# Performance work log

Hardware: AMD Instinct MI355X
Metric: run time of the kernel (lower is better)

The kernel has to match this reference:

```python
import jax, jax.numpy as jnp
import numpy as np

N, K, D, E = 30000, 20, 128, 600000


def time_encode(t, w, b):
    # TGN TimeEncode: cos(Linear(1->D)(t)) ; t: [...], returns [..., D]
    return jnp.cos(t[..., None] * w + b)


def setup_inputs() -> dict:
    key = jax.random.key(0)
    ks = jax.random.split(key, 8)
    node_features = jax.random.normal(ks[0], (N, D), dtype=jnp.float32)
    timestamps = jax.random.uniform(ks[1], (N,), dtype=jnp.float32) * 1e4
    edge_features = jax.random.normal(ks[2], (E, D), dtype=jnp.float32)
    neighbors = jax.random.randint(ks[3], (N, K), 0, N, dtype=jnp.int32)
    edge_idxs = jax.random.randint(ks[4], (N, K), 0, E, dtype=jnp.int32)
    # edge interaction times precede the query timestamps (temporal neighbor sampling)
    edge_times = jax.random.uniform(ks[5], (N, K), dtype=jnp.float32) * timestamps[:, None]
    # TGN basis-frequency init for the time encoder
    time_w = (1.0 / 10.0 ** np.linspace(0, 9, D)).astype(np.float32)
    time_w = jnp.asarray(time_w)
    time_b = jnp.zeros((D,), dtype=jnp.float32)
    s1 = 1.0 / np.sqrt(3 * D)
    W1 = jax.random.normal(ks[6], (3 * D, D), dtype=jnp.float32) * s1
    b1 = jnp.zeros((D,), dtype=jnp.float32)
    W2 = jax.random.normal(ks[7], (3 * D, D), dtype=jnp.float32) * s1
    b2 = jnp.zeros((D,), dtype=jnp.float32)
    return {"node_features": node_features, "timestamps": timestamps,
            "edge_features": edge_features, "neighbors": neighbors,
            "edge_idxs": edge_idxs, "edge_times": edge_times,
            "time_w": time_w, "time_b": time_b,
            "W1": W1, "b1": b1, "W2": W2, "b2": b2}


def reference(node_features, timestamps, edge_features, neighbors, edge_idxs,
              edge_times, time_w, time_b, W1, b1, W2, b2):
    # layer-0 neighbor embeddings = raw node features gathered at neighbor ids
    neigh_feat = node_features[neighbors]                       # [N, K, D]
    # time deltas between query time and edge times, then cosine time encoding
    deltas = timestamps[:, None] - edge_times                   # [N, K]
    edge_time_emb = time_encode(deltas, time_w, time_b)         # [N, K, D]
    edge_feat = edge_features[edge_idxs]                        # [N, K, D]
    # GraphSumEmbedding.aggregate
    neighbors_features = jnp.concatenate(
        [neigh_feat, edge_time_emb, edge_feat], axis=-1)        # [N, K, 3D]
    h = neighbors_features @ W1 + b1                            # [N, K, D]
    neighbors_sum = jax.nn.relu(jnp.sum(h, axis=1))             # [N, D]
    src_time_emb = time_encode(jnp.zeros_like(timestamps), time_w, time_b)  # [N, D]
    source_features = jnp.concatenate([node_features, src_time_emb], axis=1)
    source_embedding = jnp.concatenate([neighbors_sum, source_features], axis=1)
    return source_embedding @ W2 + b2                           # [N, D]
```

## Files before the change

### kernel.cpp

```cpp
#include <hip/hip_runtime.h>
#include <math.h>

#define DD 128
#define KNB 20
#define K3 384
#define NPB 8

typedef unsigned short u16;
typedef __attribute__((ext_vector_type(8))) short short8;
typedef __attribute__((ext_vector_type(4))) float f32x4;

static __device__ __forceinline__ u16 f2bf(float x) {
    union { float f; unsigned u; } v; v.f = x;
    unsigned r = v.u + 0x7fffu + ((v.u >> 16) & 1u);
    return (u16)(r >> 16);
}

static __device__ __forceinline__ float fcos(float x) {
    float r = x * 0.15915494309189535f;
    r = __builtin_amdgcn_fractf(r);
    return __builtin_amdgcn_cosf(r);
}

static __device__ __forceinline__ void st4bf(u16* p, float4 v) {
    ushort4 s;
    s.x = f2bf(v.x); s.y = f2bf(v.y); s.z = f2bf(v.z); s.w = f2bf(v.w);
    *(ushort4*)p = s;
}

__global__ __launch_bounds__(DD) void const_kernel(
    const float* __restrict__ tb, const float* __restrict__ W2,
    const float* __restrict__ b2, float* __restrict__ cvec)
{
    int d = threadIdx.x;
    float acc = b2[d];
    #pragma unroll 8
    for (int i = 0; i < DD; ++i)
        acc = fmaf(cosf(tb[i]), W2[(size_t)(2 * DD + i) * DD + d], acc);
    cvec[d] = acc;
}

__global__ __launch_bounds__(256) void pack_w(
    const float* __restrict__ W1, const float* __restrict__ W2,
    u16* __restrict__ W1p, u16* __restrict__ W2p)
{
    int t = blockIdx.x * 256 + threadIdx.x;
    if (t < 6144) {
        int L = t & 63;
        int ct = (t >> 6) & 7;
        int kt = t >> 9;
        int n  = ct * 16 + (L & 15);
        int kb = kt * 32 + (L >> 4) * 8;
        u16* d = W1p + (size_t)t * 8;
        #pragma unroll
        for (int j = 0; j < 8; ++j) d[j] = f2bf(W1[(size_t)(kb + j) * DD + n]);
    } else if (t < 10240) {
        int u = t - 6144;
        int L = u & 63;
        int ct = (u >> 6) & 7;
        int kt = (u >> 9) & 3;
        int part = u >> 11;
        int n  = ct * 16 + (L & 15);
        int kb = part * DD + kt * 32 + (L >> 4) * 8;
        u16* d = W2p + (size_t)u * 8;
        #pragma unroll
        for (int j = 0; j < 8; ++j) d[j] = f2bf(W2[(size_t)(kb + j) * DD + n]);
    }
}

__global__ __launch_bounds__(256) void agg_kernel(
    const float* __restrict__ nodef, const float* __restrict__ ts,
    const float* __restrict__ edgef, const int* __restrict__ neighbors,
    const int* __restrict__ edge_idxs, const float* __restrict__ edge_times,
    const float* __restrict__ tw, const float* __restrict__ tb,
    u16* __restrict__ aggbf, u16* __restrict__ nfbf, int N)
{
    __shared__ int   s_nb[NPB * KNB];
    __shared__ int   s_eg[NPB * KNB];
    __shared__ float s_dt[NPB * KNB];

    const int tid = threadIdx.x;
    const int n0  = blockIdx.x * NPB;

    if (tid < NPB * KNB) {
        int nsub = tid / KNB;
        int k    = tid - nsub * KNB;
        int nn   = n0 + nsub;
        if (nn < N) {
            s_nb[tid] = neighbors[(size_t)nn * KNB + k];
            s_eg[tid] = edge_idxs[(size_t)nn * KNB + k];
            s_dt[tid] = ts[nn] - edge_times[(size_t)nn * KNB + k];
        } else {
            s_nb[tid] = 0; s_eg[tid] = 0; s_dt[tid] = 0.f;
        }
    }
    __syncthreads();

    const int c    = tid & 31;
    const int nsub = tid >> 5;
    const int n    = n0 + nsub;

    const float4* nf4 = (const float4*)nodef;
    const float4* ef4 = (const float4*)edgef;
    const float4  w4  = ((const float4*)tw)[c];
    const float4  b4  = ((const float4*)tb)[c];

    float4 an = make_float4(0.f, 0.f, 0.f, 0.f);
    float4 ae = an, at = an;

    const int*   nb  = s_nb + nsub * KNB;
    const int*   eg  = s_eg + nsub * KNB;
    const float* dtp = s_dt + nsub * KNB;

    #pragma unroll 10
    for (int k = 0; k < KNB; ++k) {
        int   ni = nb[k];
        int   ei = eg[k];
        float dt = dtp[k];
        float4 nv = nf4[(size_t)ni * 32 + c];
        float4 ev = ef4[(size_t)ei * 32 + c];
        an.x += nv.x; an.y += nv.y; an.z += nv.z; an.w += nv.w;
        ae.x += ev.x; ae.y += ev.y; ae.z += ev.z; ae.w += ev.w;
        at.x += fcos(fmaf(dt, w4.x, b4.x));
        at.y += fcos(fmaf(dt, w4.y, b4.y));
        at.z += fcos(fmaf(dt, w4.z, b4.z));
        at.w += fcos(fmaf(dt, w4.w, b4.w));
    }

    if (n < N) {
        u16* o = aggbf + (size_t)n * K3;
        st4bf(o + 4 * c,           an);
        st4bf(o + DD + 4 * c,      at);
        st4bf(o + 2 * DD + 4 * c,  ae);
        float4 sf = nf4[(size_t)n * 32 + c];
        st4bf(nfbf + (size_t)n * DD + 4 * c, sf);
    }
}

#define APITCH 392
#define HPITCH 136

__global__ __launch_bounds__(256) void fused_gemm(
    const u16* __restrict__ aggbf, const u16* __restrict__ nfbf,
    const u16* __restrict__ W1p, const u16* __restrict__ W2p,
    const float* __restrict__ b1, const float* __restrict__ cvec,
    float* __restrict__ out, int N)
{
    __shared__ __align__(16) u16 As[32 * APITCH];

    const int tid  = threadIdx.x;
    const int lane = tid & 63;
    const int wave = tid >> 6;
    const int row0 = blockIdx.x * 32;
    const int m0     = (wave & 1) * 16;
    const int ctbase = (wave >> 1) * 4;
    const int l15  = lane & 15;
    const int quad = lane >> 4;

    {
        const float4* ag4 = (const float4*)aggbf;
        #pragma unroll
        for (int i = 0; i < 6; ++i) {
            int idx = tid + i * 256;
            int r = idx / 48, c = idx - r * 48;
            float4 v = make_float4(0.f, 0.f, 0.f, 0.f);
            int row = row0 + r;
            if (row < N) v = ag4[(size_t)row * 48 + c];
            *(float4*)&As[r * APITCH + c * 8] = v;
        }
    }
    __syncthreads();

    f32x4 acc[4];
    #pragma unroll
    for (int c = 0; c < 4; ++c) acc[c] = (f32x4){0.f, 0.f, 0.f, 0.f};

    const short8* W1v = (const short8*)W1p;
    for (int kt = 0; kt < 12; ++kt) {
        short8 a = *(const short8*)&As[(m0 + l15) * APITCH + kt * 32 + quad * 8];
        #pragma unroll
        for (int c = 0; c < 4; ++c) {
            short8 b = W1v[(size_t)(kt * 8 + ctbase + c) * 64 + lane];
            acc[c] = __builtin_amdgcn_mfma_f32_16x16x32_bf16(a, b, acc[c], 0, 0, 0);
        }
    }
    __syncthreads();

    u16* Hs  = As;
    u16* NFs = As + 32 * HPITCH;
    #pragma unroll
    for (int c = 0; c < 4; ++c) {
        int col = (ctbase + c) * 16 + l15;
        float bb = (float)KNB * b1[col];
        #pragma unroll
        for (int r = 0; r < 4; ++r) {
            float h = acc[c][r] + bb;
            h = h > 0.f ? h : 0.f;
            Hs[(m0 + quad * 4 + r) * HPITCH + col] = f2bf(h);
        }
    }
    {
        const float4* nf4 = (const float4*)nfbf;
        #pragma unroll
        for (int i = 0; i < 2; ++i) {
            int idx = tid + i * 256;
            int r = idx >> 4, c = idx & 15;
            float4 v = make_float4(0.f, 0.f, 0.f, 0.f);
            int row = row0 + r;
            if (row < N) v = nf4[(size_t)row * 16 + c];
            *(float4*)&NFs[r * HPITCH + c * 8] = v;
        }
    }
    __syncthreads();

    f32x4 acc2[4];
    #pragma unroll
    for (int c = 0; c < 4; ++c) {
        float cv = cvec[(ctbase + c) * 16 + l15];
        acc2[c] = (f32x4){cv, cv, cv, cv};
    }
    const short8* W2v = (const short8*)W2p;
    for (int kt = 0; kt < 4; ++kt) {
        short8 aH = *(const short8*)&Hs[(m0 + l15) * HPITCH + kt * 32 + quad * 8];
        #pragma unroll
        for (int c = 0; c < 4; ++c) {
            short8 b = W2v[(size_t)(kt * 8 + ctbase + c) * 64 + lane];
            acc2[c] = __builtin_amdgcn_mfma_f32_16x16x32_bf16(aH, b, acc2[c], 0, 0, 0);
        }
        short8 aN = *(const short8*)&NFs[(m0 + l15) * HPITCH + kt * 32 + quad * 8];
        #pragma unroll
        for (int c = 0; c < 4; ++c) {
            short8 b = W2v[(size_t)((4 + kt) * 8 + ctbase + c) * 64 + lane];
            acc2[c] = __builtin_amdgcn_mfma_f32_16x16x32_bf16(aN, b, acc2[c], 0, 0, 0);
        }
    }

    #pragma unroll
    for (int c = 0; c < 4; ++c) {
        int col = (ctbase + c) * 16 + l15;
        #pragma unroll
        for (int r = 0; r < 4; ++r) {
            int row = row0 + m0 + quad * 4 + r;
            if (row < N) out[(size_t)row * DD + col] = acc2[c][r];
        }
    }
}

extern "C" void kernel_launch(void* const* d_in, const int* in_sizes, int n_in,
                              void* d_out, int out_size, void* d_ws, size_t ws_size,
                              hipStream_t stream)
{
    const float* nodef      = (const float*)d_in[0];
    const float* ts         = (const float*)d_in[1];
    const float* edgef      = (const float*)d_in[2];
    const int*   neighbors  = (const int*)d_in[3];
    const int*   edge_idxs  = (const int*)d_in[4];
    const float* edge_times = (const float*)d_in[5];
    const float* tw         = (const float*)d_in[6];
    const float* tb         = (const float*)d_in[7];
    const float* W1         = (const float*)d_in[8];
    const float* b1         = (const float*)d_in[9];
    const float* W2         = (const float*)d_in[10];
    const float* b2         = (const float*)d_in[11];
    float*       out        = (float*)d_out;

    const int N = in_sizes[1];

    u16*   aggbf = (u16*)d_ws;
    u16*   nfbf  = aggbf + (size_t)N * K3;
    u16*   W1p   = nfbf + (size_t)N * DD;
    u16*   W2p   = W1p + 12 * 8 * 64 * 8;
    float* cvec  = (float*)(W2p + 2 * 4 * 8 * 64 * 8);

    hipLaunchKernelGGL(const_kernel, dim3(1), dim3(DD), 0, stream,
                       tb, W2, b2, cvec);
    hipLaunchKernelGGL(pack_w, dim3(40), dim3(256), 0, stream,
                       W1, W2, W1p, W2p);
    hipLaunchKernelGGL(agg_kernel, dim3((N + NPB - 1) / NPB), dim3(256), 0, stream,
                       nodef, ts, edgef, neighbors, edge_idxs, edge_times,
                       tw, tb, aggbf, nfbf, N);
    hipLaunchKernelGGL(fused_gemm, dim3((N + 31) / 32), dim3(256), 0, stream,
                       aggbf, nfbf, W1p, W2p, b1, cvec, out, N);
}
```

Before: 480.4 us.

## Fuse neighbor aggregation into GEMM kernel and merge weight-prep launches

The gather/aggregation stage now runs inside the GEMM kernel, writing bf16 aggregated rows straight into shared memory instead of a global workspace. The separate constant and pack kernels are merged into one launch. This removes the global round trip of the aggregated buffer and the node-feature copy, plus two launches. In exchange each block does 32 nodes of gather work before its MFMAs, and the grid shrinks from about 3750 to about 940 blocks, so there is less parallelism to hide gather latency.

```diff
diff --git a/kernel.cpp b/kernel.cpp
--- a/kernel.cpp
+++ b/kernel.cpp
@@ -4,7 +4,8 @@
 #define DD 128
 #define KNB 20
 #define K3 384
-#define NPB 8
+#define APITCH 392
+#define HPITCH 136
 
 typedef unsigned short u16;
 typedef __attribute__((ext_vector_type(8))) short short8;
@@ -28,22 +29,22 @@
     *(ushort4*)p = s;
 }
 
-__global__ __launch_bounds__(DD) void const_kernel(
-    const float* __restrict__ tb, const float* __restrict__ W2,
-    const float* __restrict__ b2, float* __restrict__ cvec)
+__global__ __launch_bounds__(256) void prep_kernel(
+    const float* __restrict__ W1, const float* __restrict__ W2,
+    const float* __restrict__ tb, const float* __restrict__ b2,
+    u16* __restrict__ W1p, u16* __restrict__ W2p, float* __restrict__ cvec)
 {
-    int d = threadIdx.x;
-    float acc = b2[d];
-    #pragma unroll 8
-    for (int i = 0; i < DD; ++i)
-        acc = fmaf(cosf(tb[i]), W2[(size_t)(2 * DD + i) * DD + d], acc);
-    cvec[d] = acc;
-}
-
-__global__ __launch_bounds__(256) void pack_w(
-    const float* __restrict__ W1, const float* __restrict__ W2,
-    u16* __restrict__ W1p, u16* __restrict__ W2p)
-{
+    if (blockIdx.x == 40) {
+        int d = threadIdx.x;
+        if (d < DD) {
+            float acc = b2[d];
+            #pragma unroll 8
+            for (int i = 0; i < DD; ++i)
+                acc = fmaf(cosf(tb[i]), W2[(size_t)(2 * DD + i) * DD + d], acc);
+            cvec[d] = acc;
+        }
+        return;
+    }
     int t = blockIdx.x * 256 + threadIdx.x;
     if (t < 6144) {
         int L = t & 63;
@@ -68,109 +69,82 @@
     }
 }
 
-__global__ __launch_bounds__(256) void agg_kernel(
+__global__ __launch_bounds__(256) void fused_all(
     const float* __restrict__ nodef, const float* __restrict__ ts,
     const float* __restrict__ edgef, const int* __restrict__ neighbors,
     const int* __restrict__ edge_idxs, const float* __restrict__ edge_times,
     const float* __restrict__ tw, const float* __restrict__ tb,
-    u16* __restrict__ aggbf, u16* __restrict__ nfbf, int N)
-{
-    __shared__ int   s_nb[NPB * KNB];
-    __shared__ int   s_eg[NPB * KNB];
-    __shared__ float s_dt[NPB * KNB];
-
-    const int tid = threadIdx.x;
-    const int n0  = blockIdx.x * NPB;
-
-    if (tid < NPB * KNB) {
-        int nsub = tid / KNB;
-        int k    = tid - nsub * KNB;
-        int nn   = n0 + nsub;
-        if (nn < N) {
-            s_nb[tid] = neighbors[(size_t)nn * KNB + k];
-            s_eg[tid] = edge_idxs[(size_t)nn * KNB + k];
-            s_dt[tid] = ts[nn] - edge_times[(size_t)nn * KNB + k];
-        } else {
-            s_nb[tid] = 0; s_eg[tid] = 0; s_dt[tid] = 0.f;
-        }
-    }
-    __syncthreads();
-
-    const int c    = tid & 31;
-    const int nsub = tid >> 5;
-    const int n    = n0 + nsub;
-
-    const float4* nf4 = (const float4*)nodef;
-    const float4* ef4 = (const float4*)edgef;
-    const float4  w4  = ((const float4*)tw)[c];
-    const float4  b4  = ((const float4*)tb)[c];
-
-    float4 an = make_float4(0.f, 0.f, 0.f, 0.f);
-    float4 ae = an, at = an;
-
-    const int*   nb  = s_nb + nsub * KNB;
-    const int*   eg  = s_eg + nsub * KNB;
-    const float* dtp = s_dt + nsub * KNB;
-
-    #pragma unroll 10
-    for (int k = 0; k < KNB; ++k) {
-        int   ni = nb[k];
-        int   ei = eg[k];
-        float dt = dtp[k];
-        float4 nv = nf4[(size_t)ni * 32 + c];
-        float4 ev = ef4[(size_t)ei * 32 + c];
-        an.x += nv.x; an.y += nv.y; an.z += nv.z; an.w += nv.w;
-        ae.x += ev.x; ae.y += ev.y; ae.z += ev.z; ae.w += ev.w;
-        at.x += fcos(fmaf(dt, w4.x, b4.x));
-        at.y += fcos(fmaf(dt, w4.y, b4.y));
-        at.z += fcos(fmaf(dt, w4.z, b4.z));
-        at.w += fcos(fmaf(dt, w4.w, b4.w));
-    }
-
-    if (n < N) {
-        u16* o = aggbf + (size_t)n * K3;
-        st4bf(o + 4 * c,           an);
-        st4bf(o + DD + 4 * c,      at);
-        st4bf(o + 2 * DD + 4 * c,  ae);
-        float4 sf = nf4[(size_t)n * 32 + c];
-        st4bf(nfbf + (size_t)n * DD + 4 * c, sf);
-    }
-}
-
-#define APITCH 392
-#define HPITCH 136
-
-__global__ __launch_bounds__(256) void fused_gemm(
-    const u16* __restrict__ aggbf, const u16* __restrict__ nfbf,
     const u16* __restrict__ W1p, const u16* __restrict__ W2p,
     const float* __restrict__ b1, const float* __restrict__ cvec,
     float* __restrict__ out, int N)
 {
-    __shared__ __align__(16) u16 As[32 * APITCH];
+    __shared__ __align__(16) u16 smem[32 * APITCH + 32 * HPITCH];
+    u16* As   = smem;
+    u16* over = smem + 32 * APITCH;
+    int*   s_nb = (int*)over;
+    int*   s_eg = s_nb + 32 * KNB;
+    float* s_dt = (float*)(s_eg + 32 * KNB);
 
     const int tid  = threadIdx.x;
+    const int row0 = blockIdx.x * 32;
+
+    for (int i = tid; i < 32 * KNB; i += 256) {
+        int nsub = i / KNB, k = i - nsub * KNB;
+        int nn = row0 + nsub;
+        if (nn < N) {
+            s_nb[i] = neighbors[(size_t)nn * KNB + k];
+            s_eg[i] = edge_idxs[(size_t)nn * KNB + k];
+            s_dt[i] = ts[nn] - edge_times[(size_t)nn * KNB + k];
+        } else { s_nb[i] = 0; s_eg[i] = 0; s_dt[i] = 0.f; }
+    }
+    __syncthreads();
+
+    {
+        const int c = tid & 31;
+        const float4* nf4 = (const float4*)nodef;
+        const float4* ef4 = (const float4*)edgef;
+        const float4  w4  = ((const float4*)tw)[c];
+        const float4  b4  = ((const float4*)tb)[c];
+
+        #pragma unroll
+        for (int g = 0; g < 4; ++g) {
+            int nsub = g * 8 + (tid >> 5);
+            int n = row0 + nsub;
+            float4 an = make_float4(0.f, 0.f, 0.f, 0.f);
+            float4 ae = an, at = an;
+            const int*   nb  = s_nb + nsub * KNB;
+            const int*   eg  = s_eg + nsub * KNB;
+            const float* dtp = s_dt + nsub * KNB;
+            int kmax = (n < N) ? KNB : 0;
+            #pragma unroll 10
+            for (int k = 0; k < kmax; ++k) {
+                int   ni = nb[k];
+                int   ei = eg[k];
+                float dt = dtp[k];
+                float4 nv = nf4[(size_t)ni * 32 + c];
+                float4 ev = ef4[(size_t)ei * 32 + c];
+                an.x += nv.x; an.y += nv.y; an.z += nv.z; an.w += nv.w;
+                ae.x += ev.x; ae.y += ev.y; ae.z += ev.z; ae.w += ev.w;
+                at.x += fcos(fmaf(dt, w4.x, b4.x));
+                at.y += fcos(fmaf(dt, w4.y, b4.y));
+                at.z += fcos(fmaf(dt, w4.z, b4.z));
+                at.w += fcos(fmaf(dt, w4.w, b4.w));
+            }
+            u16* o = As + nsub * APITCH;
+            st4bf(o + 4 * c,          an);
+            st4bf(o + DD + 4 * c,     at);
+            st4bf(o + 2 * DD + 4 * c, ae);
+        }
+    }
+    __syncthreads();
+
     const int lane = tid & 63;
     const int wave = tid >> 6;
-    const int row0 = blockIdx.x * 32;
     const int m0     = (wave & 1) * 16;
     const int ctbase = (wave >> 1) * 4;
     const int l15  = lane & 15;
     const int quad = lane >> 4;
 
-    {
-        const float4* ag4 = (const float4*)aggbf;
-        #pragma unroll
-        for (int i = 0; i < 6; ++i) {
-            int idx = tid + i * 256;
-            int r = idx / 48, c = idx - r * 48;
-            float4 v = make_float4(0.f, 0.f, 0.f, 0.f);
-            int row = row0 + r;
-            if (row < N) v = ag4[(size_t)row * 48 + c];
-            *(float4*)&As[r * APITCH + c * 8] = v;
-        }
-    }
-    __syncthreads();
-
     f32x4 acc[4];
     #pragma unroll
     for (int c = 0; c < 4; ++c) acc[c] = (f32x4){0.f, 0.f, 0.f, 0.f};
@@ -187,7 +161,7 @@
     __syncthreads();
 
     u16* Hs  = As;
-    u16* NFs = As + 32 * HPITCH;
+    u16* NFs = over;
     #pragma unroll
     for (int c = 0; c < 4; ++c) {
         int col = (ctbase + c) * 16 + l15;
@@ -200,15 +174,18 @@
         }
     }
     {
-        const float4* nf4 = (const float4*)nfbf;
+        const float4* nf4 = (const float4*)nodef;
         #pragma unroll
         for (int i = 0; i < 2; ++i) {
             int idx = tid + i * 256;
             int r = idx >> 4, c = idx & 15;
             float4 v = make_float4(0.f, 0.f, 0.f, 0.f);
             int row = row0 + r;
-            if (row < N) v = nf4[(size_t)row * 16 + c];
-            *(float4*)&NFs[r * HPITCH + c * 8] = v;
+            if (row < N) v = nf4[(size_t)row * 32 + 2 * c];
+            float4 v2 = make_float4(0.f, 0.f, 0.f, 0.f);
+            if (row < N) v2 = nf4[(size_t)row * 32 + 2 * c + 1];
+            st4bf(&NFs[r * HPITCH + c * 8],     v);
+            st4bf(&NFs[r * HPITCH + c * 8 + 4], v2);
         }
     }
     __syncthreads();
@@ -266,19 +243,13 @@
 
     const int N = in_sizes[1];
 
-    u16*   aggbf = (u16*)d_ws;
-    u16*   nfbf  = aggbf + (size_t)N * K3;
-    u16*   W1p   = nfbf + (size_t)N * DD;
-    u16*   W2p   = W1p + 12 * 8 * 64 * 8;
-    float* cvec  = (float*)(W2p + 2 * 4 * 8 * 64 * 8);
-
-    hipLaunchKernelGGL(const_kernel, dim3(1), dim3(DD), 0, stream,
-                       tb, W2, b2, cvec);
-    hipLaunchKernelGGL(pack_w, dim3(40), dim3(256), 0, stream,
-                       W1, W2, W1p, W2p);
-    hipLaunchKernelGGL(agg_kernel, dim3((N + NPB - 1) / NPB), dim3(256), 0, stream,
+    u16*   W1p  = (u16*)d_ws;
+    u16*   W2p  = W1p + 12 * 8 * 64 * 8;
+    float* cvec = (float*)(W2p + 2 * 4 * 8 * 64 * 8);
+
+    hipLaunchKernelGGL(prep_kernel, dim3(41), dim3(256), 0, stream,
+                       W1, W2, tb, b2, W1p, W2p, cvec);
+    hipLaunchKernelGGL(fused_all, dim3((N + 31) / 32), dim3(256), 0, stream,
                        nodef, ts, edgef, neighbors, edge_idxs, edge_times,
-                       tw, tb, aggbf, nfbf, N);
-    hipLaunchKernelGGL(fused_gemm, dim3((N + 31) / 32), dim3(256), 0, stream,
-                       aggbf, nfbf, W1p, W2p, b1, cvec, out, N);
-}
+                       tw, tb, W1p, W2p, b1, cvec, out, N);
+}
```

Result: no change. 489.0 us (+1.8%).
